# Performance work log

Measured on AMD Instinct MI355X. Metric: run time of the kernel, lower is better.

Reference implementation:

```python
import jax, jax.numpy as jnp
import numpy as np

B, S, HID = 4, 2048, 1024
NH = 16
HD = HID // NH  # 64


def setup_inputs() -> dict:
    key = jax.random.key(0)
    k1, k2, k3 = jax.random.split(key, 3)
    x = jax.random.normal(k1, (B, S, HID), dtype=jnp.float32)
    # causal sparse mask: True = attend
    mask = jnp.tril(jnp.ones((S, S), dtype=bool))
    w_qkv = jax.random.normal(k2, (HID, 3 * HID), dtype=jnp.float32) * 0.02
    b_qkv = jnp.zeros((3 * HID,), dtype=jnp.float32)
    w_out = jax.random.normal(k3, (HID, HID), dtype=jnp.float32) * 0.02
    b_out = jnp.zeros((HID,), dtype=jnp.float32)
    return {"x": x, "mask": mask, "w_qkv": w_qkv, "b_qkv": b_qkv,
            "w_out": w_out, "b_out": b_out}


def reference(x, mask, w_qkv, b_qkv, w_out, b_out):
    bsz, seq_len, hid = x.shape
    # QKV projection -> [B, S, H, 3*D] -> [B, H, S, 3*D]
    qkv = (x @ w_qkv + b_qkv).reshape(bsz, seq_len, NH, 3 * HD).transpose(0, 2, 1, 3)
    q, k, v = jnp.split(qkv, 3, axis=-1)  # each [B, H, S, D]
    scale = 1.0 / jnp.sqrt(jnp.asarray(HD, dtype=x.dtype))
    scores = jnp.einsum('bhqd,bhkd->bhqk', q, k) * scale
    scores = jnp.where(mask[None, None, :, :], scores, jnp.asarray(-jnp.inf, dtype=scores.dtype))
    probs = jax.nn.softmax(scores, axis=-1)
    context = jnp.einsum('bhqk,bhkd->bhqd', probs, v)  # [B, H, S, D]
    context = context.transpose(0, 2, 1, 3).reshape(bsz, seq_len, hid)
    return context @ w_out + b_out
```

## Files before the change

### kernel.cpp

```cpp
#include <hip/hip_runtime.h>
#include <stdint.h>

#define S_LEN 2048
#define NHEAD 16
#define HDIM  64
#define HIDDEN 1024
#define BATCH 4

typedef float f32x4 __attribute__((ext_vector_type(4)));
typedef __bf16 bf16x8 __attribute__((ext_vector_type(8)));
typedef unsigned short u16;

union U4B8 { uint4 u; bf16x8 b; };

__device__ __forceinline__ bf16x8 as_b8(uint4 u){ U4B8 x; x.u = u; return x.b; }

__device__ __forceinline__ f32x4 mfma16(uint4 a, uint4 b, f32x4 c){
  return __builtin_amdgcn_mfma_f32_16x16x32_bf16(as_b8(a), as_b8(b), c, 0, 0, 0);
}

__device__ __forceinline__ u16 f2bf(float f){
  __bf16 h = (__bf16)f;
  return __builtin_bit_cast(u16, h);
}

__device__ __forceinline__ float exp2fast(float x){
  return __builtin_exp2f(x);
}

__device__ __forceinline__ void gload16(const void* g, void* l){
  __builtin_amdgcn_global_load_lds(
      (const __attribute__((address_space(1))) unsigned int*)g,
      (__attribute__((address_space(3))) unsigned int*)l, 16, 0, 0);
}

#define QSCALE 0.18033688f
#define DEFER_THR 11.5f

__global__ __launch_bounds__(256) void k_cvt(const float* __restrict__ in,
                                             u16* __restrict__ out, int n4){
  int i = blockIdx.x * 256 + threadIdx.x;
  int stride = gridDim.x * 256;
  for (; i < n4; i += stride){
    float4 v = ((const float4*)in)[i];
    unsigned lo = (unsigned)f2bf(v.x) | ((unsigned)f2bf(v.y) << 16);
    unsigned hi = (unsigned)f2bf(v.z) | ((unsigned)f2bf(v.w) << 16);
    ((uint2*)out)[i] = make_uint2(lo, hi);
  }
}

__global__ __launch_bounds__(256) void k_transpose(const float* __restrict__ in,
                                                   u16* __restrict__ out,
                                                   int K, int N){
  __shared__ float t[32][33];
  int tx = threadIdx.x & 31, ty = threadIdx.x >> 5;
  int n0 = blockIdx.x * 32, k0 = blockIdx.y * 32;
  #pragma unroll
  for (int i = 0; i < 4; ++i)
    t[ty + i*8][tx] = in[(size_t)(k0 + ty + i*8) * N + n0 + tx];
  __syncthreads();
  #pragma unroll
  for (int i = 0; i < 4; ++i)
    out[(size_t)(n0 + ty + i*8) * K + k0 + tx] = f2bf(t[tx][ty + i*8]);
}

__device__ __forceinline__ void stage_gemm(
    const u16* __restrict__ A, const u16* __restrict__ Bt,
    u16* As, u16* Bs, int row0, int col0, int K, int k0, int wave, int lane)
{
  #pragma unroll
  for (int p = 0; p < 2; ++p){
    int chunk = wave * 128 + p * 64 + lane;
    int r = chunk >> 2, cseg = chunk & 3;
    const u16* ga = A  + (size_t)(row0 + r) * K + k0 + cseg * 8;
    gload16(ga, As + (size_t)(wave * 128 + p * 64) * 8);
    const u16* gb = Bt + (size_t)(col0 + r) * K + k0 + cseg * 8;
    gload16(gb, Bs + (size_t)(wave * 128 + p * 64) * 8);
  }
}

template<int MODE>
__global__ __launch_bounds__(256) void k_gemm(
    const u16* __restrict__ A, const u16* __restrict__ Bt,
    const float* __restrict__ bias,
    u16* __restrict__ oq, u16* __restrict__ ok, u16* __restrict__ ov,
    float* __restrict__ of, int M, int N, int K)
{
  __shared__ u16 As[2][128 * 32];
  __shared__ u16 Bs[2][128 * 32];
  const int tid  = threadIdx.x;
  const int wave = tid >> 6, lane = tid & 63;
  const int l4 = lane >> 4, lm = lane & 15;
  const int wr = wave >> 1, wc = wave & 1;
  const int row0 = blockIdx.y * 128;
  const int col0 = blockIdx.x * 128;

  const f32x4 fzero = {0.f, 0.f, 0.f, 0.f};
  f32x4 acc[4][4];
  #pragma unroll
  for (int m = 0; m < 4; ++m)
    #pragma unroll
    for (int n = 0; n < 4; ++n) acc[m][n] = fzero;

  stage_gemm(A, Bt, &As[0][0], &Bs[0][0], row0, col0, K, 0, wave, lane);

  const int nks = K >> 5;
  #pragma unroll 1
  for (int ks = 0; ks < nks; ++ks){
    const int cur = ks & 1;
    if (ks + 1 < nks){
      stage_gemm(A, Bt, &As[cur ^ 1][0], &Bs[cur ^ 1][0],
                 row0, col0, K, (ks + 1) << 5, wave, lane);
      asm volatile("s_waitcnt vmcnt(4)" ::: "memory");
    } else {
      asm volatile("s_waitcnt vmcnt(0)" ::: "memory");
    }
    __builtin_amdgcn_s_barrier();
    asm volatile("" ::: "memory");

    uint4 af[4], bf[4];
    #pragma unroll
    for (int m = 0; m < 4; ++m)
      af[m] = *(const uint4*)&As[cur][(wr * 64 + m * 16 + lm) * 32 + l4 * 8];
    #pragma unroll
    for (int n = 0; n < 4; ++n)
      bf[n] = *(const uint4*)&Bs[cur][(wc * 64 + n * 16 + lm) * 32 + l4 * 8];
    __builtin_amdgcn_s_setprio(1);
    #pragma unroll
    for (int m = 0; m < 4; ++m)
      #pragma unroll
      for (int n = 0; n < 4; ++n)
        acc[m][n] = mfma16(af[m], bf[n], acc[m][n]);
    __builtin_amdgcn_s_setprio(0);

    asm volatile("" ::: "memory");
    __builtin_amdgcn_s_barrier();
    asm volatile("" ::: "memory");
  }

  #pragma unroll
  for (int m = 0; m < 4; ++m){
    #pragma unroll
    for (int n = 0; n < 4; ++n){
      int c = col0 + wc * 64 + n * 16 + lm;
      float bv = bias[c];
      #pragma unroll
      for (int r = 0; r < 4; ++r){
        int row = row0 + wr * 64 + m * 16 + l4 * 4 + r;
        float val = acc[m][n][r] + bv;
        if (MODE == 0){
          int h = c / 192, e = c % 192;
          int which = e >> 6, d = e & 63;
          int b = row >> 11, s = row & 2047;
          int bh = b * 16 + h;
          if (which == 2){
            ov[((size_t)bh * HDIM + d) * S_LEN + s] = f2bf(val);
          } else {
            if (which == 0) val *= QSCALE;
            size_t idx = ((size_t)bh * S_LEN + s) * HDIM + d;
            u16* dst = (which == 0) ? oq : ok;
            dst[idx] = f2bf(val);
          }
        } else {
          of[(size_t)row * N + c] = val;
        }
      }
    }
  }
}

__device__ __forceinline__ void stage_tile8(
    const u16* __restrict__ kB, const u16* __restrict__ vB,
    u16* ldsK, u16* ldsV, int kbase, int wave, int lane)
{
  int ch  = wave * 64 + lane;
  int row = ch >> 3;
  int cc  = (ch & 7) << 4;
  int sc  = cc ^ ((row & 7) << 4);
  gload16(kB + (size_t)(kbase + row) * HDIM + (sc >> 1), ldsK + (size_t)wave * 512);
  gload16(vB + (size_t)row * S_LEN + kbase + (sc >> 1), ldsV + (size_t)wave * 512);
}

__global__ __launch_bounds__(512) void k_attn(
    const u16* __restrict__ q, const u16* __restrict__ kk,
    const u16* __restrict__ vt, u16* __restrict__ ctx)
{
  __shared__ u16 KV[2][2][64 * 64];
  __shared__ u16 Ps[8][16][72];

  const int bid = blockIdx.x;
  const int bh = bid & 63;
  const int pr = bid >> 6;
  const int wave = threadIdx.x >> 6, lane = threadIdx.x & 63;
  const int l4 = lane >> 4, lm = lane & 15;
  const size_t base = (size_t)bh * (S_LEN * HDIM);
  const u16* kB = kk + base;
  const u16* vB = vt + base;
  const int b = bh >> 4, h = bh & 15;
  const f32x4 fz = {0.f, 0.f, 0.f, 0.f};

  #pragma unroll 1
  for (int half = 0; half < 2; ++half){
    const int st = half ? (15 - pr) : pr;
    const int q0 = st * 128 + wave * 16;

    uint4 qf0, qf1;
    {
      const u16* qr = q + base + (size_t)(q0 + lm) * HDIM + l4 * 8;
      qf0 = *(const uint4*)qr;
      qf1 = *(const uint4*)(qr + 32);
    }

    float mr = -1e30f, lsp = 0.f;
    f32x4 acc[4];
    #pragma unroll
    for (int tt = 0; tt < 4; ++tt) acc[tt] = fz;

    const int nkt = 2 * st + 2;

    stage_tile8(kB, vB, &KV[0][0][0], &KV[0][1][0], 0, wave, lane);

    #pragma unroll 1
    for (int kt = 0; kt < nkt; ++kt){
      const int cur = kt & 1;
      const int kbase = kt << 6;
      if (kt + 1 < nkt){
        stage_tile8(kB, vB, &KV[cur ^ 1][0][0], &KV[cur ^ 1][1][0],
                    (kt + 1) << 6, wave, lane);
        asm volatile("s_waitcnt vmcnt(2)" ::: "memory");
      } else {
        asm volatile("s_waitcnt vmcnt(0)" ::: "memory");
      }
      __builtin_amdgcn_s_barrier();
      asm volatile("" ::: "memory");

      if (kbase < q0 + 16){
        const u16* ldsK = &KV[cur][0][0];
        const u16* ldsV = &KV[cur][1][0];

        f32x4 sv[4];
        __builtin_amdgcn_s_setprio(1);
        #pragma unroll
        for (int g = 0; g < 4; ++g){
          int rk = g * 16 + lm;
          int xa = (l4 * 16) ^ ((rk & 7) << 4);
          int xb = (64 + l4 * 16) ^ ((rk & 7) << 4);
          const u16* krow = ldsK + rk * 64;
          uint4 kf0 = *(const uint4*)(krow + (xa >> 1));
          uint4 kf1 = *(const uint4*)(krow + (xb >> 1));
          sv[g] = mfma16(kf0, qf0, fz);
          sv[g] = mfma16(kf1, qf1, sv[g]);
        }
        __builtin_amdgcn_s_setprio(0);

        if (kbase + 63 > q0){
          #pragma unroll
          for (int g = 0; g < 4; ++g)
            #pragma unroll
            for (int r = 0; r < 4; ++r){
              int kg = kbase + g * 16 + l4 * 4 + r;
              int qg = q0 + lm;
              if (kg > qg) sv[g][r] = -1e30f;
            }
        }

        float pml = sv[0][0];
        #pragma unroll
        for (int g = 0; g < 4; ++g)
          #pragma unroll
          for (int r = 0; r < 4; ++r) pml = fmaxf(pml, sv[g][r]);

        if (__any(pml > mr + DEFER_THR)){
          float pm = fmaxf(pml, __shfl_xor(pml, 16));
          pm = fmaxf(pm, __shfl_xor(pm, 32));
          float mn = fmaxf(mr, pm);
          float corr = exp2fast(mr - mn);
          mr = mn;
          lsp *= corr;
          float cf[4];
          #pragma unroll
          for (int r = 0; r < 4; ++r) cf[r] = __shfl(corr, l4 * 4 + r);
          #pragma unroll
          for (int tt = 0; tt < 4; ++tt)
            #pragma unroll
            for (int r = 0; r < 4; ++r) acc[tt][r] *= cf[r];
        }

        float s_ = 0.f;
        #pragma unroll
        for (int g = 0; g < 4; ++g){
          float p0 = exp2fast(sv[g][0] - mr);
          float p1 = exp2fast(sv[g][1] - mr);
          float p2 = exp2fast(sv[g][2] - mr);
          float p3 = exp2fast(sv[g][3] - mr);
          s_ += (p0 + p1) + (p2 + p3);
          uint2 w;
          w.x = (unsigned)f2bf(p0) | ((unsigned)f2bf(p1) << 16);
          w.y = (unsigned)f2bf(p2) | ((unsigned)f2bf(p3) << 16);
          *(uint2*)&Ps[wave][lm][g * 16 + l4 * 4] = w;
        }
        lsp += s_;

        __builtin_amdgcn_wave_barrier();
        uint4 pa0 = *(const uint4*)&Ps[wave][lm][l4 * 8];
        uint4 pa1 = *(const uint4*)&Ps[wave][lm][32 + l4 * 8];

        __builtin_amdgcn_s_setprio(1);
        #pragma unroll
        for (int tt = 0; tt < 4; ++tt){
          int rv = tt * 16 + lm;
          int xa = (l4 * 16) ^ ((rv & 7) << 4);
          int xb = (64 + l4 * 16) ^ ((rv & 7) << 4);
          const u16* vrow = ldsV + rv * 64;
          uint4 v0 = *(const uint4*)(vrow + (xa >> 1));
          uint4 v1 = *(const uint4*)(vrow + (xb >> 1));
          acc[tt] = mfma16(pa0, v0, acc[tt]);
          acc[tt] = mfma16(pa1, v1, acc[tt]);
        }
        __builtin_amdgcn_s_setprio(0);
      }

      asm volatile("" ::: "memory");
      __builtin_amdgcn_s_barrier();
      asm volatile("" ::: "memory");
    }

    lsp += __shfl_xor(lsp, 16);
    lsp += __shfl_xor(lsp, 32);
    float inv_ = 1.0f / lsp;
    float ivr[4];
    #pragma unroll
    for (int r = 0; r < 4; ++r) ivr[r] = __shfl(inv_, l4 * 4 + r);
    #pragma unroll
    for (int tt = 0; tt < 4; ++tt)
      #pragma unroll
      for (int r = 0; r < 4; ++r){
        int srow = q0 + l4 * 4 + r;
        float val = acc[tt][r] * ivr[r];
        ctx[((size_t)b * S_LEN + srow) * HIDDEN + h * HDIM + tt * 16 + lm] = f2bf(val);
      }
  }
}

extern "C" void kernel_launch(void* const* d_in, const int* in_sizes, int n_in,
                              void* d_out, int out_size, void* d_ws, size_t ws_size,
                              hipStream_t stream)
{
  const float* x     = (const float*)d_in[0];
  const float* w_qkv = (const float*)d_in[2];
  const float* b_qkv = (const float*)d_in[3];
  const float* w_out = (const float*)d_in[4];
  const float* b_out = (const float*)d_in[5];

  char* ws = (char*)d_ws;
  u16* xbf   = (u16*)(ws);
  u16* wqkvT = (u16*)(ws + 16777216);
  u16* woutT = (u16*)(ws + 23068672);
  u16* qb    = (u16*)(ws + 25165824);
  u16* kb    = (u16*)(ws + 41943040);
  u16* vb    = (u16*)(ws + 58720256);

  k_cvt<<<2048, 256, 0, stream>>>(x, xbf, (BATCH * S_LEN * HIDDEN) / 4);
  k_transpose<<<dim3(96, 32), 256, 0, stream>>>(w_qkv, wqkvT, HIDDEN, 3 * HIDDEN);
  k_transpose<<<dim3(32, 32), 256, 0, stream>>>(w_out, woutT, HIDDEN, HIDDEN);
  k_gemm<0><<<dim3(24, 64), 256, 0, stream>>>(xbf, wqkvT, b_qkv,
                                              qb, kb, vb, nullptr,
                                              BATCH * S_LEN, 3 * HIDDEN, HIDDEN);
  k_attn<<<512, 512, 0, stream>>>(qb, kb, vb, xbf);
  k_gemm<1><<<dim3(8, 64), 256, 0, stream>>>(xbf, woutT, b_out,
                                             nullptr, nullptr, nullptr,
                                             (float*)d_out, BATCH * S_LEN, HIDDEN, HIDDEN);
}
```

Before: 201.3 us.

## Swizzle GEMM LDS tiles and remap blocks per XCD for L2 locality

Loads into LDS now go through an XOR swizzle of the 16-byte segment with the row index, and the fragment reads use the matching index, so lanes reading the same column segment across rows land in different banks. The 2D grid becomes a 1D grid whose block IDs are remapped so that each XCD (bid&7) gets a contiguous band of row tiles, which should improve L2 reuse of A and B tiles. The remap assumes the grid size divides evenly by 8*nx, which holds for both launches. GEMM code outside this region is unchanged.

```diff
diff --git a/kernel.cpp b/kernel.cpp
--- a/kernel.cpp
+++ b/kernel.cpp
@@ -72,9 +72,10 @@
   for (int p = 0; p < 2; ++p){
     int chunk = wave * 128 + p * 64 + lane;
     int r = chunk >> 2, cseg = chunk & 3;
-    const u16* ga = A  + (size_t)(row0 + r) * K + k0 + cseg * 8;
+    int sseg = cseg ^ (r & 3);
+    const u16* ga = A  + (size_t)(row0 + r) * K + k0 + sseg * 8;
     gload16(ga, As + (size_t)(wave * 128 + p * 64) * 8);
-    const u16* gb = Bt + (size_t)(col0 + r) * K + k0 + cseg * 8;
+    const u16* gb = Bt + (size_t)(col0 + r) * K + k0 + sseg * 8;
     gload16(gb, Bs + (size_t)(wave * 128 + p * 64) * 8);
   }
 }
@@ -84,7 +85,7 @@
     const u16* __restrict__ A, const u16* __restrict__ Bt,
     const float* __restrict__ bias,
     u16* __restrict__ oq, u16* __restrict__ ok, u16* __restrict__ ov,
-    float* __restrict__ of, int M, int N, int K)
+    float* __restrict__ of, int M, int N, int K, int nx)
 {
   __shared__ u16 As[2][128 * 32];
   __shared__ u16 Bs[2][128 * 32];
@@ -92,8 +93,15 @@
   const int wave = tid >> 6, lane = tid & 63;
   const int l4 = lane >> 4, lm = lane & 15;
   const int wr = wave >> 1, wc = wave & 1;
-  const int row0 = blockIdx.y * 128;
-  const int col0 = blockIdx.x * 128;
+
+  const int bid = blockIdx.x;
+  const int nwg = gridDim.x;
+  const int ny8 = nwg / (8 * nx);
+  const int xcd = bid & 7, t = bid >> 3;
+  const int by = xcd * ny8 + t / nx;
+  const int bx = t % nx;
+  const int row0 = by * 128;
+  const int col0 = bx * 128;
 
   const f32x4 fzero = {0.f, 0.f, 0.f, 0.f};
   f32x4 acc[4][4];
@@ -120,11 +128,15 @@
 
     uint4 af[4], bf[4];
     #pragma unroll
-    for (int m = 0; m < 4; ++m)
-      af[m] = *(const uint4*)&As[cur][(wr * 64 + m * 16 + lm) * 32 + l4 * 8];
-    #pragma unroll
-    for (int n = 0; n < 4; ++n)
-      bf[n] = *(const uint4*)&Bs[cur][(wc * 64 + n * 16 + lm) * 32 + l4 * 8];
+    for (int m = 0; m < 4; ++m){
+      int rr = wr * 64 + m * 16 + lm;
+      af[m] = *(const uint4*)&As[cur][rr * 32 + (l4 ^ (rr & 3)) * 8];
+    }
+    #pragma unroll
+    for (int n = 0; n < 4; ++n){
+      int rr = wc * 64 + n * 16 + lm;
+      bf[n] = *(const uint4*)&Bs[cur][rr * 32 + (l4 ^ (rr & 3)) * 8];
+    }
     __builtin_amdgcn_s_setprio(1);
     #pragma unroll
     for (int m = 0; m < 4; ++m)
@@ -363,11 +375,11 @@
   k_cvt<<<2048, 256, 0, stream>>>(x, xbf, (BATCH * S_LEN * HIDDEN) / 4);
   k_transpose<<<dim3(96, 32), 256, 0, stream>>>(w_qkv, wqkvT, HIDDEN, 3 * HIDDEN);
   k_transpose<<<dim3(32, 32), 256, 0, stream>>>(w_out, woutT, HIDDEN, HIDDEN);
-  k_gemm<0><<<dim3(24, 64), 256, 0, stream>>>(xbf, wqkvT, b_qkv,
-                                              qb, kb, vb, nullptr,
-                                              BATCH * S_LEN, 3 * HIDDEN, HIDDEN);
+  k_gemm<0><<<24 * 64, 256, 0, stream>>>(xbf, wqkvT, b_qkv,
+                                         qb, kb, vb, nullptr,
+                                         BATCH * S_LEN, 3 * HIDDEN, HIDDEN, 24);
   k_attn<<<512, 512, 0, stream>>>(qb, kb, vb, xbf);
-  k_gemm<1><<<dim3(8, 64), 256, 0, stream>>>(xbf, woutT, b_out,
-                                             nullptr, nullptr, nullptr,
-                                             (float*)d_out, BATCH * S_LEN, HIDDEN, HIDDEN);
-}
+  k_gemm<1><<<8 * 64, 256, 0, stream>>>(xbf, woutT, b_out,
+                                        nullptr, nullptr, nullptr,
+                                        (float*)d_out, BATCH * S_LEN, HIDDEN, HIDDEN, 8);
+}
```

Measured after the change: 197.5 us. About the same (-1.9%).
